# Kernel tuning notes

Measured on AMD Instinct MI355X. Metric: run time of the kernel, lower is better.

The kernel has to match this reference:

```python
import jax, jax.numpy as jnp
import numpy as np

D_IN = 1024
D_OUT = 1024
N = 4096


def setup_inputs() -> dict:
    key = jax.random.key(0)
    ks = jax.random.split(key, 7)
    s_in = 1.0 / np.sqrt(D_IN)
    return {
        "x": jax.random.normal(ks[0], (N, D_IN), dtype=jnp.float32),
        "W_q": jax.random.uniform(ks[1], (D_IN, D_OUT), jnp.float32, -s_in, s_in),
        "b_q": jax.random.uniform(ks[2], (D_OUT,), jnp.float32, -s_in, s_in),
        "W_k": jax.random.uniform(ks[3], (D_IN, D_OUT), jnp.float32, -s_in, s_in),
        "b_k": jax.random.uniform(ks[4], (D_OUT,), jnp.float32, -s_in, s_in),
        "W_v": jax.random.uniform(ks[5], (D_IN, D_OUT), jnp.float32, -s_in, s_in),
        "b_v": jax.random.uniform(ks[6], (D_OUT,), jnp.float32, -s_in, s_in),
    }


def reference(x, W_q, b_q, W_k, b_k, W_v, b_v):
    # QKV projections (Linear with bias): [N, d_out]
    q = x @ W_q + b_q
    k = x @ W_k + b_k
    v = x @ W_v + b_v
    # Full attention: scores [N, N], scaled by sqrt(d_out)
    scores = (q @ k.T) / jnp.sqrt(jnp.asarray(k.shape[-1], q.dtype))
    attn = jax.nn.softmax(scores, axis=-1)
    return attn @ v  # [N, d_out]
```

## Files before the change

kernel.cpp:

```cpp
#include <hip/hip_runtime.h>

typedef __attribute__((ext_vector_type(8))) short short8;
typedef __attribute__((ext_vector_type(4))) float f32x4;
typedef __attribute__((ext_vector_type(8))) unsigned short ushort8;

typedef const unsigned int __attribute__((address_space(1)))* gas1_t;
typedef unsigned int __attribute__((address_space(3)))* las3_t;

__device__ __forceinline__ void gload_lds16(const void* g, void* l) {
  __builtin_amdgcn_global_load_lds((gas1_t)g, (las3_t)l, 16, 0, 0);
}

__device__ __forceinline__ unsigned short f2bf(float f) {
  unsigned int u = __float_as_uint(f);
  u += 0x7FFFu + ((u >> 16) & 1u);
  return (unsigned short)(u >> 16);
}
__device__ __forceinline__ float bf2f(unsigned short b) {
  return __uint_as_float(((unsigned int)b) << 16);
}

__global__ __launch_bounds__(256) void conv_f32_bf16(const float* __restrict__ in,
                                                     unsigned short* __restrict__ out, int n8) {
  int i = blockIdx.x * 256 + threadIdx.x;
  if (i >= n8) return;
  const f32x4* p = (const f32x4*)(in + (size_t)i * 8);
  f32x4 a = p[0], b = p[1];
  ushort8 o;
  o[0]=f2bf(a[0]); o[1]=f2bf(a[1]); o[2]=f2bf(a[2]); o[3]=f2bf(a[3]);
  o[4]=f2bf(b[0]); o[5]=f2bf(b[1]); o[6]=f2bf(b[2]); o[7]=f2bf(b[3]);
  *(ushort8*)(out + (size_t)i * 8) = o;
}

__global__ __launch_bounds__(256) void transconv_w(const float* __restrict__ Wq,
                                                   const float* __restrict__ Wk,
                                                   const float* __restrict__ Wv,
                                                   unsigned short* __restrict__ out) {
  __shared__ unsigned short tile[64][66];
  const float* W = (blockIdx.z == 0) ? Wq : ((blockIdx.z == 1) ? Wk : Wv);
  unsigned short* O = out + (size_t)blockIdx.z * 1048576;
  const int bi = blockIdx.x * 64;
  const int bo = blockIdx.y * 64;
#pragma unroll
  for (int p = 0; p < 16; ++p) {
    int idx = p * 256 + threadIdx.x;
    int r = idx >> 6, c = idx & 63;
    tile[r][c] = f2bf(W[(size_t)(bi + r) * 1024 + bo + c]);
  }
  __syncthreads();
#pragma unroll
  for (int p = 0; p < 16; ++p) {
    int idx = p * 256 + threadIdx.x;
    int r = idx >> 6, c = idx & 63;
    O[(size_t)(bo + r) * 1024 + bi + c] = tile[c][r];
  }
}

__global__ __launch_bounds__(256) void trans_bf16(const unsigned short* __restrict__ in,
                                                  unsigned short* __restrict__ out, int R, int C) {
  __shared__ unsigned short tile[64][66];
  const int br = blockIdx.x * 64, bc = blockIdx.y * 64;
#pragma unroll
  for (int p = 0; p < 16; ++p) {
    int idx = p * 256 + threadIdx.x;
    int r = idx >> 6, c = idx & 63;
    tile[r][c] = in[(size_t)(br + r) * C + bc + c];
  }
  __syncthreads();
#pragma unroll
  for (int p = 0; p < 16; ++p) {
    int idx = p * 256 + threadIdx.x;
    int r = idx >> 6, c = idx & 63;
    out[(size_t)(bc + r) * R + br + c] = tile[c][r];
  }
}

__global__ __launch_bounds__(256) void rowsum_rows(const unsigned short* __restrict__ E,
                                                   float* __restrict__ rsum) {
  const int tid = threadIdx.x;
  const int lane = tid & 63;
  const int w = tid >> 6;
  const unsigned short* p = E + (size_t)blockIdx.x * 4096 + tid * 16;
  ushort8 v0 = *(const ushort8*)p;
  ushort8 v1 = *(const ushort8*)(p + 8);
  float s = 0.f;
#pragma unroll
  for (int j = 0; j < 8; ++j) s += bf2f(v0[j]) + bf2f(v1[j]);
#pragma unroll
  for (int off = 32; off >= 1; off >>= 1) s += __shfl_xor(s, off);
  __shared__ float rs[4];
  if (lane == 0) rs[w] = s;
  __syncthreads();
  if (tid == 0) rsum[blockIdx.x] = rs[0] + rs[1] + rs[2] + rs[3];
}

template <int BM, int BN, int MI, int NI, int EPI>
__global__ __launch_bounds__(256, 2) void gemm_bt(
    const unsigned short* __restrict__ A, const unsigned short* __restrict__ B,
    int lda, int ldb, int K, void* __restrict__ C, int ldc,
    size_t strideBz, size_t strideCz,
    const float* __restrict__ bq, const float* __restrict__ bk, const float* __restrict__ bv,
    float scale) {
  static_assert(BM == 2 * MI * 16 && BN == 2 * NI * 16, "tile mismatch");
  __shared__ unsigned short As[2][BM * 32];
  __shared__ unsigned short Bs[2][BN * 32];
  const int tid = threadIdx.x;
  const int lane = tid & 63;
  const int w = tid >> 6;
  const int wr = w >> 1, wc = w & 1;

  const int nwgx = gridDim.x;
  const int nwg = nwgx * gridDim.y;
  const int lin = blockIdx.y * nwgx + blockIdx.x;
  const int swz = (lin & 7) * (nwg >> 3) + (lin >> 3);
  const int m0 = (swz / nwgx) * BM;
  const int n0 = (swz % nwgx) * BN;
  const int z = blockIdx.z;
  const unsigned short* Bz = B + (size_t)z * strideBz;

  f32x4 acc[MI][NI];
#pragma unroll
  for (int i = 0; i < MI; ++i)
#pragma unroll
    for (int j = 0; j < NI; ++j) acc[i][j] = f32x4{0.f, 0.f, 0.f, 0.f};

  const int l16 = lane & 15;
  const int kh = (lane >> 4) << 3;

  const unsigned short* aptr[BM / 64];
  const unsigned short* bptr[BN / 64];
#pragma unroll
  for (int i = 0; i < BM / 64; ++i) {
    int t = i * 256 + tid;
    aptr[i] = A + (size_t)(m0 + (t >> 2)) * lda + (t & 3) * 8;
  }
#pragma unroll
  for (int i = 0; i < BN / 64; ++i) {
    int t = i * 256 + tid;
    bptr[i] = Bz + (size_t)(n0 + (t >> 2)) * ldb + (t & 3) * 8;
  }

#define STAGE(buf, k0)                                                        \
  do {                                                                        \
    _Pragma("unroll") for (int _si = 0; _si < BM / 64; ++_si) {               \
      const int _st = _si * 256 + tid;                                        \
      gload_lds16(aptr[_si] + (k0), &As[buf][_st * 8]);                       \
    }                                                                         \
    _Pragma("unroll") for (int _si = 0; _si < BN / 64; ++_si) {               \
      const int _st = _si * 256 + tid;                                        \
      gload_lds16(bptr[_si] + (k0), &Bs[buf][_st * 8]);                       \
    }                                                                         \
  } while (0)

  STAGE(0, 0);
  __syncthreads();

  const int NT = K / 32;
  for (int t = 0; t < NT; ++t) {
    const int cur = t & 1;
    if (t + 1 < NT) STAGE(cur ^ 1, (t + 1) * 32);
    short8 a[MI], b[NI];
#pragma unroll
    for (int mi = 0; mi < MI; ++mi)
      a[mi] = *(const short8*)(&As[cur][(wr * (MI * 16) + mi * 16 + l16) * 32 + kh]);
#pragma unroll
    for (int ni = 0; ni < NI; ++ni)
      b[ni] = *(const short8*)(&Bs[cur][(wc * (NI * 16) + ni * 16 + l16) * 32 + kh]);
#pragma unroll
    for (int mi = 0; mi < MI; ++mi)
#pragma unroll
      for (int ni = 0; ni < NI; ++ni)
        acc[mi][ni] = __builtin_amdgcn_mfma_f32_16x16x32_bf16(a[mi], b[ni], acc[mi][ni], 0, 0, 0);
    __syncthreads();
  }
#undef STAGE

  const int row0 = m0 + wr * (MI * 16) + ((lane >> 4) << 2);
  const int col0 = n0 + wc * (NI * 16);

  float rinv[MI][4];
  if constexpr (EPI == 2) {
    const float* rsum = bq;
#pragma unroll
    for (int mi = 0; mi < MI; ++mi)
#pragma unroll
      for (int r = 0; r < 4; ++r) rinv[mi][r] = 1.0f / rsum[row0 + mi * 16 + r];
  }

#pragma unroll
  for (int mi = 0; mi < MI; ++mi) {
#pragma unroll
    for (int ni = 0; ni < NI; ++ni) {
      const int col = col0 + ni * 16 + l16;
      const int row = row0 + mi * 16;
      if constexpr (EPI == 0) {
        unsigned short* O = (unsigned short*)C + (size_t)z * strideCz;
        const float* bias = (z == 0) ? bq : ((z == 1) ? bk : bv);
        float bvv = bias[col];
#pragma unroll
        for (int r = 0; r < 4; ++r)
          O[(size_t)(row + r) * ldc + col] = f2bf(acc[mi][ni][r] + bvv);
      } else if constexpr (EPI == 1) {
        unsigned short* O = (unsigned short*)C;
#pragma unroll
        for (int r = 0; r < 4; ++r)
          O[(size_t)(row + r) * ldc + col] = f2bf(__expf(acc[mi][ni][r] * scale));
      } else {
        float* O = (float*)C;
#pragma unroll
        for (int r = 0; r < 4; ++r)
          O[(size_t)(row + r) * ldc + col] = acc[mi][ni][r] * rinv[mi][r];
      }
    }
  }
}

extern "C" void kernel_launch(void* const* d_in, const int* in_sizes, int n_in,
                              void* d_out, int out_size, void* d_ws, size_t ws_size,
                              hipStream_t stream) {
  const float* x  = (const float*)d_in[0];
  const float* Wq = (const float*)d_in[1];
  const float* bq = (const float*)d_in[2];
  const float* Wk = (const float*)d_in[3];
  const float* bk = (const float*)d_in[4];
  const float* Wv = (const float*)d_in[5];
  const float* bv = (const float*)d_in[6];
  float* out = (float*)d_out;
  char* ws = (char*)d_ws;
  const size_t MB = 1024 * 1024;

  unsigned short* xb  = (unsigned short*)(ws + 0);
  unsigned short* wt  = (unsigned short*)(ws + 8 * MB);
  float*          rsum= (float*)(ws + 8 * MB);
  unsigned short* qkv = (unsigned short*)(ws + 14 * MB);
  unsigned short* qb  = qkv;
  unsigned short* kb  = qkv + (size_t)4194304;
  unsigned short* vb  = qkv + (size_t)2 * 4194304;
  unsigned short* vt  = (unsigned short*)(ws + 38 * MB);
  unsigned short* S   = (unsigned short*)(ws + 46 * MB);

  conv_f32_bf16<<<2048, 256, 0, stream>>>(x, xb, 524288);
  transconv_w<<<dim3(16, 16, 3), 256, 0, stream>>>(Wq, Wk, Wv, wt);
  gemm_bt<128, 128, 4, 4, 0><<<dim3(8, 32, 3), 256, 0, stream>>>(
      xb, wt, 1024, 1024, 1024, qkv, 1024,
      (size_t)1048576, (size_t)4194304, bq, bk, bv, 1.0f);
  trans_bf16<<<dim3(64, 16), 256, 0, stream>>>(vb, vt, 4096, 1024);
  gemm_bt<128, 128, 4, 4, 1><<<dim3(32, 32), 256, 0, stream>>>(
      qb, kb, 1024, 1024, 1024, S, 4096,
      (size_t)0, (size_t)0, nullptr, nullptr, nullptr, 0.03125f);
  rowsum_rows<<<4096, 256, 0, stream>>>(S, rsum);
  gemm_bt<128, 64, 4, 2, 2><<<dim3(16, 32), 256, 0, stream>>>(
      S, vt, 4096, 4096, 4096, out, 1024,
      (size_t)0, (size_t)0, rsum, nullptr, nullptr, 1.0f);
}
```

Measured before the change: 162.7 us.

## Fuse softmax rowsum into score GEMM and split-K the PV GEMM with atomics

Drops the separate rowsum kernel. The exp-score GEMM epilogue now reduces each row's bf16 exp values across lanes and adds them into rsum with atomics. The final S·V GEMM changes from a 128x64 tile over full K=4096 to 128x128 tiles split four ways along K, with partial results atomically added into a zeroed output. Two memsets are added. The aim is to save a full pass over the 32MB S matrix and give the last GEMM more parallelism, at the cost of float atomics on the output and on rsum.

```diff
diff --git a/kernel.cpp b/kernel.cpp
--- a/kernel.cpp
+++ b/kernel.cpp
@@ -75,32 +75,13 @@
   }
 }
 
-__global__ __launch_bounds__(256) void rowsum_rows(const unsigned short* __restrict__ E,
-                                                   float* __restrict__ rsum) {
-  const int tid = threadIdx.x;
-  const int lane = tid & 63;
-  const int w = tid >> 6;
-  const unsigned short* p = E + (size_t)blockIdx.x * 4096 + tid * 16;
-  ushort8 v0 = *(const ushort8*)p;
-  ushort8 v1 = *(const ushort8*)(p + 8);
-  float s = 0.f;
-#pragma unroll
-  for (int j = 0; j < 8; ++j) s += bf2f(v0[j]) + bf2f(v1[j]);
-#pragma unroll
-  for (int off = 32; off >= 1; off >>= 1) s += __shfl_xor(s, off);
-  __shared__ float rs[4];
-  if (lane == 0) rs[w] = s;
-  __syncthreads();
-  if (tid == 0) rsum[blockIdx.x] = rs[0] + rs[1] + rs[2] + rs[3];
-}
-
 template <int BM, int BN, int MI, int NI, int EPI>
 __global__ __launch_bounds__(256, 2) void gemm_bt(
     const unsigned short* __restrict__ A, const unsigned short* __restrict__ B,
     int lda, int ldb, int K, void* __restrict__ C, int ldc,
     size_t strideBz, size_t strideCz,
     const float* __restrict__ bq, const float* __restrict__ bk, const float* __restrict__ bv,
-    float scale) {
+    float scale, float* __restrict__ rsum) {
   static_assert(BM == 2 * MI * 16 && BN == 2 * NI * 16, "tile mismatch");
   __shared__ unsigned short As[2][BM * 32];
   __shared__ unsigned short Bs[2][BN * 32];
@@ -117,6 +98,7 @@
   const int n0 = (swz % nwgx) * BN;
   const int z = blockIdx.z;
   const unsigned short* Bz = B + (size_t)z * strideBz;
+  const size_t koff = (EPI == 2) ? (size_t)z * K : 0;
 
   f32x4 acc[MI][NI];
 #pragma unroll
@@ -132,12 +114,12 @@
 #pragma unroll
   for (int i = 0; i < BM / 64; ++i) {
     int t = i * 256 + tid;
-    aptr[i] = A + (size_t)(m0 + (t >> 2)) * lda + (t & 3) * 8;
+    aptr[i] = A + (size_t)(m0 + (t >> 2)) * lda + koff + (t & 3) * 8;
   }
 #pragma unroll
   for (int i = 0; i < BN / 64; ++i) {
     int t = i * 256 + tid;
-    bptr[i] = Bz + (size_t)(n0 + (t >> 2)) * ldb + (t & 3) * 8;
+    bptr[i] = Bz + (size_t)(n0 + (t >> 2)) * ldb + koff + (t & 3) * 8;
   }
 
 #define STAGE(buf, k0)                                                        \
@@ -178,40 +160,63 @@
   const int row0 = m0 + wr * (MI * 16) + ((lane >> 4) << 2);
   const int col0 = n0 + wc * (NI * 16);
 
-  float rinv[MI][4];
-  if constexpr (EPI == 2) {
-    const float* rsum = bq;
-#pragma unroll
-    for (int mi = 0; mi < MI; ++mi)
-#pragma unroll
-      for (int r = 0; r < 4; ++r) rinv[mi][r] = 1.0f / rsum[row0 + mi * 16 + r];
-  }
-
-#pragma unroll
-  for (int mi = 0; mi < MI; ++mi) {
-#pragma unroll
-    for (int ni = 0; ni < NI; ++ni) {
-      const int col = col0 + ni * 16 + l16;
-      const int row = row0 + mi * 16;
-      if constexpr (EPI == 0) {
-        unsigned short* O = (unsigned short*)C + (size_t)z * strideCz;
-        const float* bias = (z == 0) ? bq : ((z == 1) ? bk : bv);
+  if constexpr (EPI == 0) {
+    unsigned short* O = (unsigned short*)C + (size_t)z * strideCz;
+    const float* bias = (z == 0) ? bq : ((z == 1) ? bk : bv);
+#pragma unroll
+    for (int mi = 0; mi < MI; ++mi)
+#pragma unroll
+      for (int ni = 0; ni < NI; ++ni) {
+        const int col = col0 + ni * 16 + l16;
+        const int row = row0 + mi * 16;
         float bvv = bias[col];
 #pragma unroll
         for (int r = 0; r < 4; ++r)
           O[(size_t)(row + r) * ldc + col] = f2bf(acc[mi][ni][r] + bvv);
-      } else if constexpr (EPI == 1) {
-        unsigned short* O = (unsigned short*)C;
+      }
+  } else if constexpr (EPI == 1) {
+    unsigned short* O = (unsigned short*)C;
+#pragma unroll
+    for (int mi = 0; mi < MI; ++mi) {
+      float rs[4] = {0.f, 0.f, 0.f, 0.f};
+      const int row = row0 + mi * 16;
+#pragma unroll
+      for (int ni = 0; ni < NI; ++ni) {
+        const int col = col0 + ni * 16 + l16;
+#pragma unroll
+        for (int r = 0; r < 4; ++r) {
+          unsigned short ub = f2bf(__expf(acc[mi][ni][r] * scale));
+          O[(size_t)(row + r) * ldc + col] = ub;
+          rs[r] += bf2f(ub);
+        }
+      }
+#pragma unroll
+      for (int off = 1; off <= 8; off <<= 1) {
+#pragma unroll
+        for (int r = 0; r < 4; ++r) rs[r] += __shfl_xor(rs[r], off);
+      }
+      if (l16 == 0) {
+#pragma unroll
+        for (int r = 0; r < 4; ++r) unsafeAtomicAdd(&rsum[row + r], rs[r]);
+      }
+    }
+  } else {
+    float* O = (float*)C;
+    float rinv[MI][4];
+#pragma unroll
+    for (int mi = 0; mi < MI; ++mi)
+#pragma unroll
+      for (int r = 0; r < 4; ++r) rinv[mi][r] = 1.0f / rsum[row0 + mi * 16 + r];
+#pragma unroll
+    for (int mi = 0; mi < MI; ++mi)
+#pragma unroll
+      for (int ni = 0; ni < NI; ++ni) {
+        const int col = col0 + ni * 16 + l16;
+        const int row = row0 + mi * 16;
 #pragma unroll
         for (int r = 0; r < 4; ++r)
-          O[(size_t)(row + r) * ldc + col] = f2bf(__expf(acc[mi][ni][r] * scale));
-      } else {
-        float* O = (float*)C;
-#pragma unroll
-        for (int r = 0; r < 4; ++r)
-          O[(size_t)(row + r) * ldc + col] = acc[mi][ni][r] * rinv[mi][r];
-      }
-    }
+          unsafeAtomicAdd(&O[(size_t)(row + r) * ldc + col], acc[mi][ni][r] * rinv[mi][r]);
+      }
   }
 }
 
@@ -239,17 +244,18 @@
   unsigned short* vt  = (unsigned short*)(ws + 38 * MB);
   unsigned short* S   = (unsigned short*)(ws + 46 * MB);
 
+  hipMemsetAsync(out, 0, (size_t)out_size * sizeof(float), stream);
   conv_f32_bf16<<<2048, 256, 0, stream>>>(x, xb, 524288);
   transconv_w<<<dim3(16, 16, 3), 256, 0, stream>>>(Wq, Wk, Wv, wt);
   gemm_bt<128, 128, 4, 4, 0><<<dim3(8, 32, 3), 256, 0, stream>>>(
       xb, wt, 1024, 1024, 1024, qkv, 1024,
-      (size_t)1048576, (size_t)4194304, bq, bk, bv, 1.0f);
+      (size_t)1048576, (size_t)4194304, bq, bk, bv, 1.0f, nullptr);
+  hipMemsetAsync(rsum, 0, 4096 * sizeof(float), stream);
   trans_bf16<<<dim3(64, 16), 256, 0, stream>>>(vb, vt, 4096, 1024);
   gemm_bt<128, 128, 4, 4, 1><<<dim3(32, 32), 256, 0, stream>>>(
       qb, kb, 1024, 1024, 1024, S, 4096,
-      (size_t)0, (size_t)0, nullptr, nullptr, nullptr, 0.03125f);
-  rowsum_rows<<<4096, 256, 0, stream>>>(S, rsum);
-  gemm_bt<128, 64, 4, 2, 2><<<dim3(16, 32), 256, 0, stream>>>(
-      S, vt, 4096, 4096, 4096, out, 1024,
-      (size_t)0, (size_t)0, rsum, nullptr, nullptr, 1.0f);
-}
+      (size_t)0, (size_t)0, nullptr, nullptr, nullptr, 0.03125f, rsum);
+  gemm_bt<128, 128, 4, 4, 2><<<dim3(8, 32, 4), 256, 0, stream>>>(
+      S, vt, 4096, 4096, 1024, out, 1024,
+      (size_t)0, (size_t)0, nullptr, nullptr, nullptr, 1.0f, rsum);
+}
```

New measurement: 187.7 us. 15.4% more time.
